# Kernel tuning notes

Measured on AMD Instinct MI355X. Metric: run time of the kernel, lower is better.

The kernel has to match this reference:

```python
import jax, jax.numpy as jnp
import numpy as np

NUM_EMBED = 1024
NUM_HEADS = 16
BLOCK_SIZE = 2048


def setup_inputs() -> dict:
    key = jax.random.key(0)
    k1, k2, k3, k4, k5 = jax.random.split(key, 5)
    C = NUM_EMBED
    s = 1.0 / np.sqrt(C)
    x = jax.random.normal(k1, (2, BLOCK_SIZE, C), dtype=jnp.float32)
    # nn.Linear params: weight (out,in), bias (out,)
    w_attn = jax.random.uniform(k2, (3 * C, C), minval=-s, maxval=s, dtype=jnp.float32)
    b_attn = jax.random.uniform(k3, (3 * C,), minval=-s, maxval=s, dtype=jnp.float32)
    w_proj = jax.random.uniform(k4, (C, C), minval=-s, maxval=s, dtype=jnp.float32)
    b_proj = jax.random.uniform(k5, (C,), minval=-s, maxval=s, dtype=jnp.float32)
    return {"x": x, "w_attn": w_attn, "b_attn": b_attn, "w_proj": w_proj, "b_proj": b_proj}


def reference(x, w_attn, b_attn, w_proj, b_proj):
    B, T, C = x.shape
    H = NUM_HEADS
    D = C // H
    kqv = jnp.einsum('btc,oc->bto', x, w_attn) + b_attn  # (B,T,3C)
    # Original code splits as K, Q, V in that order.
    K, Q, V = jnp.split(kqv, 3, axis=2)
    K = K.reshape(B, T, H, D).transpose(0, 2, 1, 3)  # (B,H,T,D)
    Q = Q.reshape(B, T, H, D).transpose(0, 2, 1, 3)
    V = V.reshape(B, T, H, D).transpose(0, 2, 1, 3)
    aff = jnp.einsum('bhqd,bhkd->bhqk', Q, K) * (D ** -0.5)  # (B,H,T,T)
    causal = jnp.tril(jnp.ones((T, T), dtype=bool))
    aff = jnp.where(causal[None, None], aff, jnp.float32(-jnp.inf))
    wei = jax.nn.softmax(aff, axis=-1)
    attn = jnp.einsum('bhqk,bhkd->bhqd', wei, V)
    attn = attn.transpose(0, 2, 1, 3).reshape(B, T, C)
    out = jnp.einsum('btc,oc->bto', attn, w_proj) + b_proj
    return out
```

## Files before the change

### kernel.cpp

```cpp
#include <hip/hip_runtime.h>
#include <hip/hip_bf16.h>
#include <cstdint>

typedef __attribute__((ext_vector_type(8))) short bf16x8;
typedef __attribute__((ext_vector_type(4))) float f32x4;
typedef __attribute__((ext_vector_type(16))) float f32x16;
typedef __attribute__((ext_vector_type(4))) uint16_t u16x4;

__device__ __forceinline__ uint16_t f2b(float f) {
  union { float f; uint32_t i; } v; v.f = f;
  return (uint16_t)((v.i + 0x7FFFu + ((v.i >> 16) & 1u)) >> 16);
}

__device__ __forceinline__ uint32_t pkbf(float a, float b) {
  union { __hip_bfloat162 h2; uint32_t u; } c;
  c.h2 = __float22bfloat162_rn(make_float2(a, b));
  return c.u;
}

#define GLDS16(g, l) __builtin_amdgcn_global_load_lds( \
    (const __attribute__((address_space(1))) void*)(g), \
    (__attribute__((address_space(3))) void*)(l), 16, 0, 0)

__global__ __launch_bounds__(256) void cvt_all(
    const float* __restrict__ x, const float* __restrict__ wa, const float* __restrict__ wp,
    uint16_t* __restrict__ xb, uint16_t* __restrict__ wab, uint16_t* __restrict__ wpb) {
  const int i = (blockIdx.x * 256 + threadIdx.x) * 4;
  const float* src; uint16_t* dst; int off;
  if (i < 4194304)      { src = x;  dst = xb;  off = i; }
  else if (i < 7340032) { src = wa; dst = wab; off = i - 4194304; }
  else                  { src = wp; dst = wpb; off = i - 7340032; }
  const float4 v = *(const float4*)(src + off);
  u16x4 o;
  o.x = f2b(v.x); o.y = f2b(v.y); o.z = f2b(v.z); o.w = f2b(v.w);
  *(u16x4*)(dst + off) = o;
}

template <int BM, int BN, bool OUT_BF16>
__global__ __launch_bounds__(256) void gemm_bt_bias(
    const uint16_t* __restrict__ A, const uint16_t* __restrict__ B,
    const float* __restrict__ bias, void* __restrict__ Cv,
    int M, int N, int K) {
  constexpr int MI = BM / 32;
  constexpr int NJ = BN / 32;
  constexpr int CA = BM / 16;
  constexpr int CB = BN / 16;
  constexpr int CPW = (2 * (CA + CB)) / 4;
  constexpr size_t CT_BYTES = OUT_BF16 ? (size_t)4 * (BM / 2) * 72 * 2 : 0;
  constexpr size_t ST_BYTES = (size_t)2 * (BM * 32 + BN * 32) * 2;
  constexpr size_t LB = CT_BYTES > ST_BYTES ? CT_BYTES : ST_BYTES;
  __shared__ alignas(16) unsigned char ldsb[LB];
  uint16_t* lds = (uint16_t*)ldsb;
  const int offB0 = BM * 32;
  const int offA1 = BM * 32 + BN * 32;
  const int offB1 = 2 * BM * 32 + BN * 32;

  const int tid = threadIdx.x;
  const int wave = tid >> 6, lane = tid & 63;
  const int q4 = lane >> 4, l16 = lane & 15;
  const int wm = wave >> 1, wn = wave & 1;
  const long blockM = (long)blockIdx.y * BM;
  const long blockN = (long)blockIdx.x * BN;

  f32x4 acc[MI][NJ] = {};

  for (int k0 = 0; k0 < K; k0 += 64) {
#pragma unroll
    for (int c = 0; c < CPW; ++c) {
      const int id = c * 4 + wave;
      const uint16_t* mat; long rowBase; int a, kk, off;
      if (id < CA)                { mat = A; rowBase = blockM; a = id;             kk = k0;      off = 0; }
      else if (id < CA + CB)      { mat = B; rowBase = blockN; a = id - CA;        kk = k0;      off = offB0; }
      else if (id < 2 * CA + CB)  { mat = A; rowBase = blockM; a = id - CA - CB;   kk = k0 + 32; off = offA1; }
      else                        { mat = B; rowBase = blockN; a = id - 2*CA - CB; kk = k0 + 32; off = offB1; }
      const int flat = a * 64 + lane;
      const int row = flat >> 2, seg = flat & 3;
      GLDS16(mat + (rowBase + row) * (long)K + kk + seg * 8, lds + off + a * 512);
    }
    __syncthreads();
#pragma unroll
    for (int h = 0; h < 2; ++h) {
      const uint16_t* Ah = lds + (h ? offA1 : 0);
      const uint16_t* Bh = lds + (h ? offB1 : offB0);
      bf16x8 af[MI], bfr[NJ];
#pragma unroll
      for (int i = 0; i < MI; ++i)
        af[i] = *(const bf16x8*)&Ah[(wm * (BM / 2) + i * 16 + l16) * 32 + q4 * 8];
#pragma unroll
      for (int j = 0; j < NJ; ++j)
        bfr[j] = *(const bf16x8*)&Bh[(wn * (BN / 2) + j * 16 + l16) * 32 + q4 * 8];
#pragma unroll
      for (int i = 0; i < MI; ++i)
#pragma unroll
        for (int j = 0; j < NJ; ++j)
          acc[i][j] = __builtin_amdgcn_mfma_f32_16x16x32_bf16(af[i], bfr[j], acc[i][j], 0, 0, 0);
    }
    __syncthreads();
  }

  if constexpr (OUT_BF16) {
    uint16_t* ct = lds + wave * (BM / 2) * 72;
#pragma unroll
    for (int j = 0; j < NJ; ++j) {
      const float bv = bias[blockN + wn * (BN / 2) + j * 16 + l16];
#pragma unroll
      for (int i = 0; i < MI; ++i)
#pragma unroll
        for (int r = 0; r < 4; ++r)
          ct[(i * 16 + q4 * 4 + r) * 72 + j * 16 + l16] = f2b(acc[i][j][r] + bv);
    }
    __syncthreads();
    uint16_t* Cb = (uint16_t*)Cv;
#pragma unroll
    for (int st = 0; st < BM / 16; ++st) {
      const int flat = st * 64 + lane;
      const int row = flat >> 3, seg = flat & 7;
      const bf16x8 v = *(const bf16x8*)&ct[row * 72 + seg * 8];
      *(bf16x8*)&Cb[(blockM + wm * (BM / 2) + row) * (long)N + blockN + wn * 64 + seg * 8] = v;
    }
  } else {
    float* Cb = (float*)Cv;
#pragma unroll
    for (int j = 0; j < NJ; ++j) {
      const long col = blockN + wn * (BN / 2) + j * 16 + l16;
      const float bv = bias[col];
#pragma unroll
      for (int i = 0; i < MI; ++i)
#pragma unroll
        for (int r = 0; r < 4; ++r) {
          const long row = blockM + wm * (BM / 2) + i * 16 + q4 * 4 + r;
          Cb[row * (long)N + col] = acc[i][j][r] + bv;
        }
    }
  }
}

__global__ __launch_bounds__(256, 2) void attn_flash(
    const uint16_t* __restrict__ kqv, uint16_t* __restrict__ attn) {
  constexpr int T = 2048, C = 1024, C3 = 3072;
  __shared__ alignas(16) unsigned char ldsb[35840];
  uint16_t* KP = (uint16_t*)ldsb;
  uint16_t* Vt = (uint16_t*)(ldsb + 18432);
  uint32_t* VtW = (uint32_t*)(ldsb + 18432);
  float* mlb  = (float*)ldsb;
  float* obuf = (float*)(ldsb + 1024);

  const int tid = threadIdx.x;
  const int wave = tid >> 6, lane = tid & 63;
  const int l32 = lane & 31, hh = lane >> 5;
  const int sidx = blockIdx.x >> 5, bh = blockIdx.x & 31;
  const int b = bh >> 4, h = bh & 15;
  const size_t base = (size_t)b * T * C3;
  const int hD = h * 64;
  const int lr = lane >> 3, kch = lane & 7;
  const float sc = 0.125f * 1.4426950408889634f;

  const int qb = 31 - sidx;
  const int dd = qb * 64 + 63 - wave * 32;
  const int nktw = (dd < 0) ? 0 : ((dd >> 7) + 1);

  bf16x8 qf[2][4];
#pragma unroll
  for (int qc = 0; qc < 2; ++qc)
#pragma unroll
    for (int m = 0; m < 4; ++m)
      qf[qc][m] = *(const bf16x8*)&kqv[base + (size_t)(qb * 64 + qc * 32 + l32) * C3 + C + hD + m * 16 + hh * 8];

  f32x16 o[2][2] = {};
  float m_i[2] = {-1e30f, -1e30f}, l_i[2] = {0.f, 0.f};

  bf16x8 pk[4], pv0[2], pv1[2];
  if (nktw > 0) {
    const int kb0 = wave * 32;
#pragma unroll
    for (int rr = 0; rr < 4; ++rr)
      pk[rr] = *(const bf16x8*)&kqv[base + (size_t)(kb0 + rr * 8 + lr) * C3 + hD + kch * 8];
#pragma unroll
    for (int s2 = 0; s2 < 2; ++s2) {
      const size_t gg = base + (size_t)(kb0 + 2 * (s2 * 8 + lr)) * C3 + 2 * C + hD + kch * 8;
      pv0[s2] = *(const bf16x8*)&kqv[gg];
      pv1[s2] = *(const bf16x8*)&kqv[gg + C3];
    }
  }

  for (int kt = 0; kt < nktw; ++kt) {
    const int key0 = kt * 128 + wave * 32;
#pragma unroll
    for (int rr = 0; rr < 4; ++rr)
      *(bf16x8*)&KP[(wave * 32 + rr * 8 + lr) * 72 + kch * 8] = pk[rr];
#pragma unroll
    for (int s2 = 0; s2 < 2; ++s2) {
      const int colw = (wave * 16 + s2 * 8 + lr + 8 * kch) & 63;
      const uint32_t* a0 = (const uint32_t*)&pv0[s2];
      const uint32_t* a1 = (const uint32_t*)&pv1[s2];
#pragma unroll
      for (int i = 0; i < 8; ++i) {
        const uint32_t w = (i & 1)
            ? __builtin_amdgcn_perm(a1[i >> 1], a0[i >> 1], 0x07060302u)
            : __builtin_amdgcn_perm(a1[i >> 1], a0[i >> 1], 0x05040100u);
        VtW[(kch * 8 + i) * 68 + colw] = w;
      }
    }
    if (kt + 1 < nktw) {
      const int kb2 = (kt + 1) * 128 + wave * 32;
#pragma unroll
      for (int rr = 0; rr < 4; ++rr)
        pk[rr] = *(const bf16x8*)&kqv[base + (size_t)(kb2 + rr * 8 + lr) * C3 + hD + kch * 8];
#pragma unroll
      for (int s2 = 0; s2 < 2; ++s2) {
        const size_t gg = base + (size_t)(kb2 + 2 * (s2 * 8 + lr)) * C3 + 2 * C + hD + kch * 8;
        pv0[s2] = *(const bf16x8*)&kqv[gg];
        pv1[s2] = *(const bf16x8*)&kqv[gg + C3];
      }
    }

    bf16x8 kf[4];
#pragma unroll
    for (int m = 0; m < 4; ++m)
      kf[m] = *(const bf16x8*)&KP[(wave * 32 + l32) * 72 + m * 16 + hh * 8];

#pragma unroll
    for (int qc = 0; qc < 2; ++qc) {
      if (key0 > qb * 64 + qc * 32 + 31) continue;
      f32x16 z = {};
#pragma unroll
      for (int m = 0; m < 4; ++m)
        z = __builtin_amdgcn_mfma_f32_32x32x16_bf16(kf[m], qf[qc][m], z, 0, 0, 0);
      if (key0 + 31 > qb * 64 + qc * 32) {
        const int qg = qb * 64 + qc * 32 + l32;
#pragma unroll
        for (int r = 0; r < 16; ++r) {
          const int kg = key0 + (r & 3) + 8 * (r >> 2) + 4 * hh;
          if (kg > qg) z[r] = -1e30f;
        }
      }
      float t8[8];
#pragma unroll
      for (int r = 0; r < 8; ++r) t8[r] = fmaxf(z[r], z[r + 8]);
#pragma unroll
      for (int r = 0; r < 4; ++r) t8[r] = fmaxf(t8[r], t8[r + 4]);
      float mloc = fmaxf(fmaxf(t8[0], t8[1]), fmaxf(t8[2], t8[3]));
      mloc = fmaxf(mloc, __shfl_xor(mloc, 32, 64));
      const float pm = fmaxf(mloc * sc, -3.0e4f);
      if (__any(pm - m_i[qc] > 8.0f)) {
        const float mnew = fmaxf(m_i[qc], pm);
        const float alpha = exp2f(m_i[qc] - mnew);
#pragma unroll
        for (int r = 0; r < 16; ++r) {
          const float ar = __shfl(alpha, (r & 3) + 8 * (r >> 2) + 4 * hh, 64);
          o[qc][0][r] *= ar;
          o[qc][1][r] *= ar;
        }
        l_i[qc] *= alpha;
        m_i[qc] = mnew;
      }
#pragma unroll
      for (int r = 0; r < 16; ++r)
        z[r] = exp2f(fmaf(z[r], sc, -m_i[qc]));
      float s8[8];
#pragma unroll
      for (int r = 0; r < 8; ++r) s8[r] = z[r] + z[r + 8];
#pragma unroll
      for (int r = 0; r < 4; ++r) s8[r] += s8[r + 4];
      float rs = (s8[0] + s8[1]) + (s8[2] + s8[3]);
      rs += __shfl_xor(rs, 32, 64);
      l_i[qc] += rs;

      uint32_t x0 = pkbf(z[0], z[1]),   x1 = pkbf(z[2], z[3]);
      uint32_t y0 = pkbf(z[4], z[5]),   y1 = pkbf(z[6], z[7]);
      uint32_t x2 = pkbf(z[8], z[9]),   x3 = pkbf(z[10], z[11]);
      uint32_t y2 = pkbf(z[12], z[13]), y3 = pkbf(z[14], z[15]);
      asm volatile("v_permlane32_swap_b32 %0, %1" : "+v"(x0), "+v"(y0));
      asm volatile("v_permlane32_swap_b32 %0, %1" : "+v"(x1), "+v"(y1));
      asm volatile("v_permlane32_swap_b32 %0, %1" : "+v"(x2), "+v"(y2));
      asm volatile("v_permlane32_swap_b32 %0, %1" : "+v"(x3), "+v"(y3));
#pragma unroll
      for (int cc = 0; cc < 2; ++cc) {
        union { bf16x8 v; uint32_t w[4]; } pa;
        if (cc == 0) { pa.w[0] = x0; pa.w[1] = x1; pa.w[2] = y0; pa.w[3] = y1; }
        else         { pa.w[0] = x2; pa.w[1] = x3; pa.w[2] = y2; pa.w[3] = y3; }
#pragma unroll
        for (int db = 0; db < 2; ++db) {
          const int d = db * 32 + l32;
          const int col = (wave * 32 + cc * 16 + hh * 8 + 16 * (d >> 3)) & 127;
          const bf16x8 vf = *(const bf16x8*)&Vt[d * 136 + col];
          o[qc][db] = __builtin_amdgcn_mfma_f32_32x32x16_bf16(pa.v, vf, o[qc][db], 0, 0, 0);
        }
      }
    }
  }

#pragma unroll
  for (int qc = 0; qc < 2; ++qc) {
    __syncthreads();
    if (hh == 0) {
      mlb[wave * 64 + l32] = m_i[qc];
      mlb[wave * 64 + 32 + l32] = l_i[qc];
    }
#pragma unroll
    for (int r = 0; r < 16; ++r) {
      const int ql = (r & 3) + 8 * (r >> 2) + 4 * hh;
      const int bw = wave * 2112 + ql * 66 + l32;
      obuf[bw] = o[qc][0][r];
      obuf[bw + 32] = o[qc][1][r];
    }
    __syncthreads();
    float mw[4], lw[4];
#pragma unroll
    for (int w = 0; w < 4; ++w) {
      mw[w] = mlb[w * 64 + l32];
      lw[w] = mlb[w * 64 + 32 + l32];
    }
    const float M = fmaxf(fmaxf(mw[0], mw[1]), fmaxf(mw[2], mw[3]));
    float L = 0.f, ww[4];
#pragma unroll
    for (int w = 0; w < 4; ++w) { ww[w] = exp2f(mw[w] - M); L += lw[w] * ww[w]; }
    const float Li = 1.0f / L;
    const int cb = wave * 2 + hh;
    float acc[8] = {};
#pragma unroll
    for (int w = 0; w < 4; ++w)
#pragma unroll
      for (int p = 0; p < 4; ++p) {
        const float2 v = *(const float2*)&obuf[w * 2112 + l32 * 66 + cb * 8 + p * 2];
        acc[2 * p]     += v.x * ww[w];
        acc[2 * p + 1] += v.y * ww[w];
      }
    union { bf16x8 v; uint32_t w4[4]; } ov;
#pragma unroll
    for (int p = 0; p < 4; ++p)
      ov.w4[p] = pkbf(acc[2 * p] * Li, acc[2 * p + 1] * Li);
    *(bf16x8*)&attn[((size_t)b * T + qb * 64 + qc * 32 + l32) * C + hD + cb * 8] = ov.v;
  }
}

extern "C" void kernel_launch(void* const* d_in, const int* in_sizes, int n_in,
                              void* d_out, int out_size, void* d_ws, size_t ws_size,
                              hipStream_t stream) {
  const float* x      = (const float*)d_in[0];
  const float* w_attn = (const float*)d_in[1];
  const float* b_attn = (const float*)d_in[2];
  const float* w_proj = (const float*)d_in[3];
  const float* b_proj = (const float*)d_in[4];
  float* out = (float*)d_out;

  uint16_t* xb    = (uint16_t*)d_ws;
  uint16_t* wab   = xb  + (size_t)4096 * 1024;
  uint16_t* wpb   = wab + (size_t)3072 * 1024;
  uint16_t* kqv   = wpb + (size_t)1024 * 1024;
  uint16_t* attnb = kqv + (size_t)4096 * 3072;

  dim3 blk(256, 1, 1);
  hipLaunchKernelGGL(cvt_all, dim3(8192), blk, 0, stream, x, w_attn, w_proj, xb, wab, wpb);

  hipLaunchKernelGGL((gemm_bt_bias<128, 128, true>), dim3(3072 / 128, 4096 / 128, 1), blk, 0, stream,
                     xb, wab, b_attn, (void*)kqv, 4096, 3072, 1024);
  hipLaunchKernelGGL(attn_flash, dim3(1024, 1, 1), blk, 0, stream, kqv, attnb);
  hipLaunchKernelGGL((gemm_bt_bias<128, 64, false>), dim3(1024 / 64, 4096 / 128, 1), blk, 0, stream,
                     attnb, wpb, b_proj, (void*)out, 4096, 1024, 1024);
}
```

Measured before the change: 190.3 us.

## Pipeline GEMM K-loop with triple-buffered async LDS loads

Replaces the load-then-compute K loop in the bias GEMM with a three-stage ring buffer of 32-wide K slices. Each stage is issued two iterations ahead via global_load_lds, and explicit vmcnt waits plus raw barriers hide global latency behind MFMA work. It also raises MFMA wave priority and adds occupancy hints to launch bounds. The costs are more LDS per block, hand-tuned vmcnt counts that depend on the per-wave load count, and a single barrier guarding ring-slot reuse.

```diff
diff --git a/kernel.cpp b/kernel.cpp
--- a/kernel.cpp
+++ b/kernel.cpp
@@ -21,6 +21,8 @@
 #define GLDS16(g, l) __builtin_amdgcn_global_load_lds( \
     (const __attribute__((address_space(1))) void*)(g), \
     (__attribute__((address_space(3))) void*)(l), 16, 0, 0)
+
+#define VMW(n) asm volatile("s_waitcnt vmcnt(" #n ")" ::: "memory")
 
 __global__ __launch_bounds__(256) void cvt_all(
     const float* __restrict__ x, const float* __restrict__ wa, const float* __restrict__ wp,
@@ -37,7 +39,7 @@
 }
 
 template <int BM, int BN, bool OUT_BF16>
-__global__ __launch_bounds__(256) void gemm_bt_bias(
+__global__ __launch_bounds__(256, BN == 128 ? 3 : 4) void gemm_bt_bias(
     const uint16_t* __restrict__ A, const uint16_t* __restrict__ B,
     const float* __restrict__ bias, void* __restrict__ Cv,
     int M, int N, int K) {
@@ -45,15 +47,14 @@
   constexpr int NJ = BN / 32;
   constexpr int CA = BM / 16;
   constexpr int CB = BN / 16;
-  constexpr int CPW = (2 * (CA + CB)) / 4;
+  constexpr int CPW = (CA + CB) / 4;
+  constexpr int ABLK = BM * 32;
+  constexpr int BUFSZ = (BM + BN) * 32;
+  constexpr size_t ST_BYTES = (size_t)3 * BUFSZ * 2;
   constexpr size_t CT_BYTES = OUT_BF16 ? (size_t)4 * (BM / 2) * 72 * 2 : 0;
-  constexpr size_t ST_BYTES = (size_t)2 * (BM * 32 + BN * 32) * 2;
   constexpr size_t LB = CT_BYTES > ST_BYTES ? CT_BYTES : ST_BYTES;
   __shared__ alignas(16) unsigned char ldsb[LB];
   uint16_t* lds = (uint16_t*)ldsb;
-  const int offB0 = BM * 32;
-  const int offA1 = BM * 32 + BN * 32;
-  const int offB1 = 2 * BM * 32 + BN * 32;
 
   const int tid = threadIdx.x;
   const int wave = tid >> 6, lane = tid & 63;
@@ -61,42 +62,57 @@
   const int wm = wave >> 1, wn = wave & 1;
   const long blockM = (long)blockIdx.y * BM;
   const long blockN = (long)blockIdx.x * BN;
+  const int NK = K >> 5;
 
   f32x4 acc[MI][NJ] = {};
 
-  for (int k0 = 0; k0 < K; k0 += 64) {
+  auto STAGE = [&](int s) {
+    uint16_t* buf = lds + (s % 3) * BUFSZ;
 #pragma unroll
     for (int c = 0; c < CPW; ++c) {
       const int id = c * 4 + wave;
-      const uint16_t* mat; long rowBase; int a, kk, off;
-      if (id < CA)                { mat = A; rowBase = blockM; a = id;             kk = k0;      off = 0; }
-      else if (id < CA + CB)      { mat = B; rowBase = blockN; a = id - CA;        kk = k0;      off = offB0; }
-      else if (id < 2 * CA + CB)  { mat = A; rowBase = blockM; a = id - CA - CB;   kk = k0 + 32; off = offA1; }
-      else                        { mat = B; rowBase = blockN; a = id - 2*CA - CB; kk = k0 + 32; off = offB1; }
+      const uint16_t* mat; long rowBase; int a, off;
+      if (id < CA) { mat = A; rowBase = blockM; a = id;      off = a * 512; }
+      else         { mat = B; rowBase = blockN; a = id - CA; off = ABLK + a * 512; }
       const int flat = a * 64 + lane;
       const int row = flat >> 2, seg = flat & 3;
-      GLDS16(mat + (rowBase + row) * (long)K + kk + seg * 8, lds + off + a * 512);
-    }
-    __syncthreads();
-#pragma unroll
-    for (int h = 0; h < 2; ++h) {
-      const uint16_t* Ah = lds + (h ? offA1 : 0);
-      const uint16_t* Bh = lds + (h ? offB1 : offB0);
-      bf16x8 af[MI], bfr[NJ];
-#pragma unroll
-      for (int i = 0; i < MI; ++i)
-        af[i] = *(const bf16x8*)&Ah[(wm * (BM / 2) + i * 16 + l16) * 32 + q4 * 8];
+      GLDS16(mat + (rowBase + row) * (long)K + s * 32 + seg * 8, buf + off);
+    }
+  };
+
+  STAGE(0);
+  STAGE(1);
+  for (int s = 0; s < NK; ++s) {
+    if (s + 2 < NK) STAGE(s + 2);
+    __builtin_amdgcn_sched_barrier(0);
+    if (s + 2 < NK) {
+      if constexpr (CPW == 4) VMW(8); else VMW(6);
+    } else if (s + 2 == NK) {
+      if constexpr (CPW == 4) VMW(4); else VMW(3);
+    } else {
+      VMW(0);
+    }
+    __builtin_amdgcn_sched_barrier(0);
+    __builtin_amdgcn_s_barrier();
+    const uint16_t* Ah = lds + (s % 3) * BUFSZ;
+    const uint16_t* Bh = Ah + ABLK;
+    bf16x8 af[MI], bfr[NJ];
+#pragma unroll
+    for (int i = 0; i < MI; ++i)
+      af[i] = *(const bf16x8*)&Ah[(wm * (BM / 2) + i * 16 + l16) * 32 + q4 * 8];
+#pragma unroll
+    for (int j = 0; j < NJ; ++j)
+      bfr[j] = *(const bf16x8*)&Bh[(wn * (BN / 2) + j * 16 + l16) * 32 + q4 * 8];
+    __builtin_amdgcn_s_setprio(1);
+#pragma unroll
+    for (int i = 0; i < MI; ++i)
 #pragma unroll
       for (int j = 0; j < NJ; ++j)
-        bfr[j] = *(const bf16x8*)&Bh[(wn * (BN / 2) + j * 16 + l16) * 32 + q4 * 8];
-#pragma unroll
-      for (int i = 0; i < MI; ++i)
-#pragma unroll
-        for (int j = 0; j < NJ; ++j)
-          acc[i][j] = __builtin_amdgcn_mfma_f32_16x16x32_bf16(af[i], bfr[j], acc[i][j], 0, 0, 0);
-    }
-    __syncthreads();
-  }
+        acc[i][j] = __builtin_amdgcn_mfma_f32_16x16x32_bf16(af[i], bfr[j], acc[i][j], 0, 0, 0);
+    __builtin_amdgcn_s_setprio(0);
+    __builtin_amdgcn_s_barrier();
+  }
+  __syncthreads();
 
   if constexpr (OUT_BF16) {
     uint16_t* ct = lds + wave * (BM / 2) * 72;
```

Result: faster. 186.4 us (-2.1%).
